# Optimization experiments

Measured on AMD Instinct MI355X. Metric: run time of the kernel, lower is better.

The kernel has to match this reference:

```python
import jax, jax.numpy as jnp
import numpy as np

HIDDEN = 1024
N_HEAD = 16
HEAD_DIM = HIDDEN // N_HEAD  # 64
BATCH = 1
SEQ = 4096
THETA = 10000.0


def _rope_cos_sin(seq_len, head_dim, dtype=jnp.float32):
    # freqs[t, j] = t / theta^(2j/dim), j in [0, dim/2)
    inv_freq = 1.0 / (THETA ** (jnp.arange(0, head_dim, 2, dtype=dtype) / head_dim))
    t = jnp.arange(seq_len, dtype=dtype)
    freqs = jnp.outer(t, inv_freq)           # [S, D/2]
    return jnp.cos(freqs), jnp.sin(freqs)


def _apply_rope(x, cos, sin):
    # x: [B, S, H, D]; pairs (x[...,2j], x[...,2j+1]) rotated by angle freqs[t, j]
    x2 = x.reshape(*x.shape[:-1], -1, 2)       # [B, S, H, D/2, 2]
    x_re, x_im = x2[..., 0], x2[..., 1]
    c = cos[None, :, None, :]                   # [1, S, 1, D/2]
    s = sin[None, :, None, :]
    out_re = x_re * c - x_im * s
    out_im = x_re * s + x_im * c
    out = jnp.stack([out_re, out_im], axis=-1)  # [B, S, H, D/2, 2]
    return out.reshape(x.shape)


def setup_inputs() -> dict:
    key = jax.random.key(0)
    kx, kq, kk, kv = jax.random.split(key, 4)
    scale = 1.0 / np.sqrt(HIDDEN)
    return {
        "x": jax.random.normal(kx, (BATCH, SEQ, HIDDEN), dtype=jnp.float32),
        "wq": jax.random.normal(kq, (HIDDEN, HIDDEN), dtype=jnp.float32) * scale,
        "wk": jax.random.normal(kk, (HIDDEN, HIDDEN), dtype=jnp.float32) * scale,
        "wv": jax.random.normal(kv, (HIDDEN, HIDDEN), dtype=jnp.float32) * scale,
    }


def reference(x, wq, wk, wv):
    B, S, _ = x.shape
    # torch nn.Linear(no bias): y = x @ W.T
    xq = (x @ wq.T).reshape(B, S, N_HEAD, HEAD_DIM).astype(jnp.float32)
    xk = (x @ wk.T).reshape(B, S, N_HEAD, HEAD_DIM).astype(jnp.float32)
    xv = (x @ wv.T).reshape(B, S, N_HEAD, HEAD_DIM).astype(jnp.float32)

    cos, sin = _rope_cos_sin(S, HEAD_DIM)
    q = _apply_rope(xq, cos, sin)
    k = _apply_rope(xk, cos, sin)

    # [B, H, S, S] scores, no causal mask (matches source)
    scores = jnp.einsum("bqhd,bkhd->bhqk", q, k) / jnp.sqrt(
        jnp.asarray(HEAD_DIM, dtype=q.dtype))
    attn = jax.nn.softmax(scores, axis=-1)
    out = jnp.einsum("bhqk,bkhd->bqhd", attn, xv)  # [B, S, H, D]
    return out.reshape(B, S, N_HEAD * HEAD_DIM)
```

## Files before the change

kernel.cpp:

```cpp
#include <hip/hip_runtime.h>
#include <stdint.h>


#define SEQLEN 4096
#define NHEAD 16
#define HDIM 64

typedef __bf16 bf16x8 __attribute__((ext_vector_type(8)));
typedef float f32x4 __attribute__((ext_vector_type(4)));
typedef float f32x16 __attribute__((ext_vector_type(16)));

__device__ __forceinline__ unsigned short f2bf(float f) {
  union { float f; unsigned int u; } v; v.f = f;
  unsigned int r = v.u + 0x7FFFu + ((v.u >> 16) & 1u);
  return (unsigned short)(r >> 16);
}
__device__ __forceinline__ unsigned int pkc(float lo, float hi) {
  union { __bf16 b[2]; unsigned int u; } z;
  z.b[0] = (__bf16)lo; z.b[1] = (__bf16)hi;
  return z.u;
}
__device__ __forceinline__ bf16x8 as_bf(uint4 v) { return __builtin_bit_cast(bf16x8, v); }
__device__ __forceinline__ f32x4 mfma16(bf16x8 a, bf16x8 b, f32x4 c) {
  return __builtin_amdgcn_mfma_f32_16x16x32_bf16(a, b, c, 0, 0, 0);
}
__device__ __forceinline__ f32x16 mfma32(bf16x8 a, bf16x8 b, f32x16 c) {
  return __builtin_amdgcn_mfma_f32_32x32x16_bf16(a, b, c, 0, 0, 0);
}

__global__ __launch_bounds__(256) void k_convert(
    const float* __restrict__ x, const float* __restrict__ wq,
    const float* __restrict__ wk, const float* __restrict__ wv,
    unsigned short* __restrict__ xbf, unsigned short* __restrict__ wbf) {
  int i = blockIdx.x * 256 + threadIdx.x;
  const int NX = SEQLEN * 1024 / 4;
  const int NW = 1024 * 1024 / 4;
  float4 v;
  unsigned short* dst;
  int di;
  if (i < NX) {
    v = ((const float4*)x)[i]; dst = xbf; di = i;
  } else {
    int j = i - NX;
    const float4* src = (const float4*)((j < NW) ? wq : (j < 2 * NW) ? wk : wv);
    v = src[j & (NW - 1)];
    dst = wbf; di = j;
  }
  ushort4 o; o.x = f2bf(v.x); o.y = f2bf(v.y); o.z = f2bf(v.z); o.w = f2bf(v.w);
  ((ushort4*)dst)[di] = o;
}

__global__ __launch_bounds__(256) void k_table(float* __restrict__ ct, float* __restrict__ st) {
  int i = blockIdx.x * 256 + threadIdx.x;
  int s = i >> 5, j = i & 31;
  double inv = exp(-(double)j * 0.28782313662425572);
  double a = (double)s * inv;
  ct[i] = (float)cos(a);
  st[i] = (float)sin(a);
}

__global__ __launch_bounds__(256) void k_gemm(
    const unsigned short* __restrict__ xbf, const unsigned short* __restrict__ wbf,
    const float* __restrict__ ct, const float* __restrict__ st,
    unsigned short* __restrict__ qbf, unsigned short* __restrict__ kbf,
    unsigned short* __restrict__ vT) {
  __shared__ __align__(16) unsigned short As[2][128 * 40];
  __shared__ __align__(16) unsigned short Bs[2][128 * 40];
  const int t = threadIdx.x;
  const int bn = blockIdx.x, bm = blockIdx.y;
  const int lane = t & 63, wave = t >> 6;
  const int r = lane & 15, g = lane >> 4;
  const int wm = wave >> 1, wn = wave & 1;

  const int c0 = t, c1 = t + 256;
  const int ar0 = c0 >> 2, ao0 = (c0 & 3) * 16;
  const int ar1 = c1 >> 2, ao1 = (c1 & 3) * 16;
  const char* Ab = (const char*)xbf;
  const char* Bb = (const char*)wbf;

  uint4 ra0, ra1, rb0, rb1;
#define LD_TILE(kk)                                                             \
  ra0 = *(const uint4*)(Ab + (size_t)(bm * 128 + ar0) * 2048 + (kk) * 64 + ao0); \
  ra1 = *(const uint4*)(Ab + (size_t)(bm * 128 + ar1) * 2048 + (kk) * 64 + ao1); \
  rb0 = *(const uint4*)(Bb + (size_t)(bn * 128 + ar0) * 2048 + (kk) * 64 + ao0); \
  rb1 = *(const uint4*)(Bb + (size_t)(bn * 128 + ar1) * 2048 + (kk) * 64 + ao1);

  LD_TILE(0)
  f32x4 zero4 = {0.f, 0.f, 0.f, 0.f};
  f32x4 acc[4][4];
#pragma unroll
  for (int m = 0; m < 4; ++m)
#pragma unroll
    for (int n = 0; n < 4; ++n) acc[m][n] = zero4;

  for (int kk = 0; kk < 32; ++kk) {
    unsigned short* Ac = As[kk & 1];
    unsigned short* Bc = Bs[kk & 1];
    *(uint4*)((char*)Ac + ar0 * 80 + ao0) = ra0;
    *(uint4*)((char*)Ac + ar1 * 80 + ao1) = ra1;
    *(uint4*)((char*)Bc + ar0 * 80 + ao0) = rb0;
    *(uint4*)((char*)Bc + ar1 * 80 + ao1) = rb1;
    __syncthreads();
    if (kk < 31) { LD_TILE(kk + 1) }
    bf16x8 af[4], bfr[4];
#pragma unroll
    for (int m = 0; m < 4; ++m)
      af[m] = as_bf(*(const uint4*)((const char*)Ac + (wm * 64 + m * 16 + r) * 80 + g * 16));
#pragma unroll
    for (int n = 0; n < 4; ++n)
      bfr[n] = as_bf(*(const uint4*)((const char*)Bc + (wn * 64 + n * 16 + r) * 80 + g * 16));
#pragma unroll
    for (int m = 0; m < 4; ++m)
#pragma unroll
      for (int n = 0; n < 4; ++n)
        acc[m][n] = mfma16(af[m], bfr[n], acc[m][n]);
  }

  const int matid = bn >> 3;
#pragma unroll
  for (int m = 0; m < 4; ++m) {
    const int row0 = bm * 128 + wm * 64 + m * 16 + 4 * g;
#pragma unroll
    for (int n = 0; n < 4; ++n) {
      const int col = bn * 128 + wn * 64 + n * 16 + r;
      const int d = col & 63;
      const int hh = (col >> 6) & 15;
      if (matid < 2) {
        const int jdx = (col >> 1) & 31;
        const float sgn = (col & 1) ? 1.0f : -1.0f;
        unsigned short* dst = (matid == 0) ? qbf : kbf;
        const float qs = (matid == 0) ? 0.18033688011112042f : 1.0f;
#pragma unroll
        for (int j = 0; j < 4; ++j) {
          float v = acc[m][n][j];
          float p = __shfl_xor(v, 1);
          int srow = row0 + j;
          float cv = ct[srow * 32 + jdx];
          float sv = st[srow * 32 + jdx];
          float o = (v * cv + p * sv * sgn) * qs;
          dst[(size_t)srow * 1024 + (hh * 64 + d)] = f2bf(o);
        }
      } else {
        ushort4 o;
        o.x = f2bf(acc[m][n][0]); o.y = f2bf(acc[m][n][1]);
        o.z = f2bf(acc[m][n][2]); o.w = f2bf(acc[m][n][3]);
        *(ushort4*)&vT[((size_t)(hh * 64 + d)) * SEQLEN + row0] = o;
      }
    }
  }
}

__global__ __launch_bounds__(256) void k_attn(
    const unsigned short* __restrict__ qbf, const unsigned short* __restrict__ kbf,
    const unsigned short* __restrict__ vT, float* __restrict__ out) {
  __shared__ __align__(16) char smem[32768];
  const int t = threadIdx.x;
  const int b = blockIdx.x;
  const int work = (b & 7) * 64 + (b >> 3);
  const int h = work >> 5;
  const int qb = work & 31;
  const int lane = t & 63, qw = t >> 6;
  const int li = lane & 31, hi = lane >> 5;
  const int q0 = qb * 128 + qw * 32;

  bf16x8 qf[4];
#pragma unroll
  for (int c = 0; c < 4; ++c)
    qf[c] = as_bf(*(const uint4*)((const char*)qbf +
              (size_t)(q0 + li) * 2048 + h * 128 + c * 32 + hi * 16));

  f32x16 z16 = {0.f};
  f32x16 acc[2];
  acc[0] = z16; acc[1] = z16;
  f32x16 accL = z16;

  uint4 onesu; onesu.x = 0x3F803F80u; onesu.y = 0x3F803F80u;
  onesu.z = 0x3F803F80u; onesu.w = 0x3F803F80u;
  const bf16x8 ones8 = as_bf(onesu);

  const int srow = t >> 2, sbyte = (t & 3) * 16;
  const int swz = (srow & 7) << 4;
  const int wa0 = srow * 128 + (sbyte ^ swz);
  const int wa1 = srow * 128 + ((sbyte + 64) ^ swz);
  const char* kg = (const char*)kbf + h * 128;
  const char* vg = (const char*)vT + (size_t)h * HDIM * SEQLEN * 2;

  uint4 rk0, rk1, rv0, rv1;
#define LD_KV64(kt)                                                            \
  rk0 = *(const uint4*)(kg + (size_t)((kt) * 64 + srow) * 2048 + sbyte);       \
  rk1 = *(const uint4*)(kg + (size_t)((kt) * 64 + srow) * 2048 + sbyte + 64);  \
  rv0 = *(const uint4*)(vg + (size_t)srow * 8192 + (kt) * 128 + sbyte);        \
  rv1 = *(const uint4*)(vg + (size_t)srow * 8192 + (kt) * 128 + sbyte + 64);

  LD_KV64(0)

  const int frsw = (lane & 7) << 4;

  for (int j = 0; j < 64; ++j) {
    char* Kb = smem + (j & 1) * 8192;
    char* Vb = smem + 16384 + (j & 1) * 8192;
    *(uint4*)(Kb + wa0) = rk0;
    *(uint4*)(Kb + wa1) = rk1;
    *(uint4*)(Vb + wa0) = rv0;
    *(uint4*)(Vb + wa1) = rv1;
    __syncthreads();
    if (j < 63) { LD_KV64(j + 1) }

    f32x16 sT[2];
    sT[0] = z16; sT[1] = z16;
    __builtin_amdgcn_s_setprio(1);
#pragma unroll
    for (int c = 0; c < 4; ++c) {
      const int co = (((2 * c + hi) * 16) ^ frsw);
      bf16x8 k0 = as_bf(*(const uint4*)(Kb + li * 128 + co));
      bf16x8 k1 = as_bf(*(const uint4*)(Kb + (32 + li) * 128 + co));
      sT[0] = mfma32(k0, qf[c], sT[0]);
      sT[1] = mfma32(k1, qf[c], sT[1]);
    }
    __builtin_amdgcn_s_setprio(0);

    bf16x8 vf[2][4];
#pragma unroll
    for (int dt = 0; dt < 2; ++dt) {
      const int vrow = (dt * 32 + li) * 128;
#pragma unroll
      for (int kc = 0; kc < 4; ++kc) {
        uint2 vlo = *(const uint2*)(Vb + vrow + (((kc * 32) ^ frsw) + hi * 8));
        uint2 vhi = *(const uint2*)(Vb + vrow + (((kc * 32 + 16) ^ frsw) + hi * 8));
        uint4 vv; vv.x = vlo.x; vv.y = vlo.y; vv.z = vhi.x; vv.w = vhi.y;
        vf[dt][kc] = as_bf(vv);
      }
    }

#pragma unroll
    for (int s = 0; s < 2; ++s)
#pragma unroll
      for (int i = 0; i < 16; ++i) sT[s][i] = __builtin_amdgcn_exp2f(sT[s][i]);

    bf16x8 pfr[4];
#pragma unroll
    for (int kc = 0; kc < 4; ++kc) {
      const int sub = kc >> 1, bix = (kc & 1) * 8;
      uint4 bw;
      bw.x = pkc(sT[sub][bix + 0], sT[sub][bix + 1]);
      bw.y = pkc(sT[sub][bix + 2], sT[sub][bix + 3]);
      bw.z = pkc(sT[sub][bix + 4], sT[sub][bix + 5]);
      bw.w = pkc(sT[sub][bix + 6], sT[sub][bix + 7]);
      pfr[kc] = as_bf(bw);
    }
    __builtin_amdgcn_s_setprio(1);
#pragma unroll
    for (int kc = 0; kc < 4; ++kc) {
      acc[0] = mfma32(vf[0][kc], pfr[kc], acc[0]);
      acc[1] = mfma32(vf[1][kc], pfr[kc], acc[1]);
      accL = mfma32(ones8, pfr[kc], accL);
    }
    __builtin_amdgcn_s_setprio(0);
  }

  float linv = 1.0f / accL[0];

  __syncthreads();
  float* eb = (float*)smem + qw * 1056;
#pragma unroll
  for (int dt = 0; dt < 2; ++dt) {
#pragma unroll
    for (int i = 0; i < 16; ++i)
      eb[li * 33 + ((i & 3) + 8 * (i >> 2) + 4 * hi)] = acc[dt][i] * linv;
    __asm__ volatile("" ::: "memory");
#pragma unroll
    for (int it = 0; it < 16; ++it) {
      int q = it * 2 + hi;
      float v = eb[q * 33 + li];
      out[(size_t)(q0 + q) * 1024 + h * 64 + dt * 32 + li] = v;
    }
    __asm__ volatile("" ::: "memory");
  }
}

extern "C" void kernel_launch(void* const* d_in, const int* in_sizes, int n_in,
                              void* d_out, int out_size, void* d_ws, size_t ws_size,
                              hipStream_t stream) {
  const float* x  = (const float*)d_in[0];
  const float* wq = (const float*)d_in[1];
  const float* wk = (const float*)d_in[2];
  const float* wv = (const float*)d_in[3];
  float* out = (float*)d_out;
  char* ws = (char*)d_ws;

  unsigned short* qbf = (unsigned short*)(ws);
  unsigned short* kbf = (unsigned short*)(ws + ((size_t)8 << 20));
  unsigned short* vT  = (unsigned short*)(ws + ((size_t)16 << 20));
  unsigned short* xbf = (unsigned short*)(ws + ((size_t)24 << 20));
  unsigned short* wbf = (unsigned short*)(ws + ((size_t)32 << 20));
  float* ct = (float*)(ws + ((size_t)38 << 20));
  float* st = (float*)(ws + ((size_t)38 << 20) + ((size_t)512 << 10));

  k_convert<<<dim3(7168), dim3(256), 0, stream>>>(x, wq, wk, wv, xbf, wbf);
  k_table<<<dim3(512), dim3(256), 0, stream>>>(ct, st);
  k_gemm<<<dim3(24, 32), dim3(256), 0, stream>>>(xbf, wbf, ct, st, qbf, kbf, vT);
  k_attn<<<dim3(512), dim3(256), 0, stream>>>(qbf, kbf, vT, out);
}
```

Measured before the change: 170.3 us.

## Split attention KV range in two halves and combine partials in a new kernel

Each attention block now handles only half of the key/value sequence, which doubles the grid from 512 to 1024 blocks. Each half writes an unnormalized output tile and its row sums to workspace. A new elementwise kernel adds the two partials and divides by the summed denominators. The aim is more blocks per CU and better latency hiding, at the cost of an extra launch and extra global traffic to write and re-read the partial outputs.

```diff
diff --git a/kernel.cpp b/kernel.cpp
--- a/kernel.cpp
+++ b/kernel.cpp
@@ -152,13 +152,15 @@
 
 __global__ __launch_bounds__(256) void k_attn(
     const unsigned short* __restrict__ qbf, const unsigned short* __restrict__ kbf,
-    const unsigned short* __restrict__ vT, float* __restrict__ out) {
+    const unsigned short* __restrict__ vT, float* __restrict__ po0,
+    float* __restrict__ out, float* __restrict__ pl) {
   __shared__ __align__(16) char smem[32768];
   const int t = threadIdx.x;
   const int b = blockIdx.x;
-  const int work = (b & 7) * 64 + (b >> 3);
-  const int h = work >> 5;
-  const int qb = work & 31;
+  const int work = (b & 7) * 128 + (b >> 3);
+  const int h = work >> 6;
+  const int qb = (work >> 1) & 31;
+  const int hf = work & 1;
   const int lane = t & 63, qw = t >> 6;
   const int li = lane & 31, hi = lane >> 5;
   const int q0 = qb * 128 + qw * 32;
@@ -192,11 +194,11 @@
   rv0 = *(const uint4*)(vg + (size_t)srow * 8192 + (kt) * 128 + sbyte);        \
   rv1 = *(const uint4*)(vg + (size_t)srow * 8192 + (kt) * 128 + sbyte + 64);
 
-  LD_KV64(0)
+  LD_KV64(hf * 32)
 
   const int frsw = (lane & 7) << 4;
 
-  for (int j = 0; j < 64; ++j) {
+  for (int j = 0; j < 32; ++j) {
     char* Kb = smem + (j & 1) * 8192;
     char* Vb = smem + 16384 + (j & 1) * 8192;
     *(uint4*)(Kb + wa0) = rk0;
@@ -204,7 +206,7 @@
     *(uint4*)(Vb + wa0) = rv0;
     *(uint4*)(Vb + wa1) = rv1;
     __syncthreads();
-    if (j < 63) { LD_KV64(j + 1) }
+    if (j < 31) { LD_KV64(hf * 32 + j + 1) }
 
     f32x16 sT[2];
     sT[0] = z16; sT[1] = z16;
@@ -258,7 +260,8 @@
     __builtin_amdgcn_s_setprio(0);
   }
 
-  float linv = 1.0f / accL[0];
+  float* pout = hf ? out : po0;
+  if (hi == 0) pl[hf * 65536 + h * 4096 + q0 + li] = accL[0];
 
   __syncthreads();
   float* eb = (float*)smem + qw * 1056;
@@ -266,16 +269,33 @@
   for (int dt = 0; dt < 2; ++dt) {
 #pragma unroll
     for (int i = 0; i < 16; ++i)
-      eb[li * 33 + ((i & 3) + 8 * (i >> 2) + 4 * hi)] = acc[dt][i] * linv;
+      eb[li * 33 + ((i & 3) + 8 * (i >> 2) + 4 * hi)] = acc[dt][i];
     __asm__ volatile("" ::: "memory");
 #pragma unroll
     for (int it = 0; it < 16; ++it) {
       int q = it * 2 + hi;
       float v = eb[q * 33 + li];
-      out[(size_t)(q0 + q) * 1024 + h * 64 + dt * 32 + li] = v;
+      pout[(size_t)(q0 + q) * 1024 + h * 64 + dt * 32 + li] = v;
     }
     __asm__ volatile("" ::: "memory");
   }
+}
+
+__global__ __launch_bounds__(256) void k_combine(
+    const float* __restrict__ po, const float* __restrict__ pl,
+    float* __restrict__ out) {
+  int i = blockIdx.x * 256 + threadIdx.x;
+  int flat = i << 2;
+  int q = flat >> 10;
+  int h = (flat >> 6) & 15;
+  float l = pl[h * 4096 + q] + pl[65536 + h * 4096 + q];
+  float linv = 1.0f / l;
+  float4 o = ((const float4*)out)[i];
+  float4 p = ((const float4*)po)[i];
+  float4 r;
+  r.x = (o.x + p.x) * linv; r.y = (o.y + p.y) * linv;
+  r.z = (o.z + p.z) * linv; r.w = (o.w + p.w) * linv;
+  ((float4*)out)[i] = r;
 }
 
 extern "C" void kernel_launch(void* const* d_in, const int* in_sizes, int n_in,
@@ -295,9 +315,12 @@
   unsigned short* wbf = (unsigned short*)(ws + ((size_t)32 << 20));
   float* ct = (float*)(ws + ((size_t)38 << 20));
   float* st = (float*)(ws + ((size_t)38 << 20) + ((size_t)512 << 10));
+  float* po0 = (float*)(ws + ((size_t)24 << 20));
+  float* pl  = (float*)(ws + ((size_t)40 << 20));
 
   k_convert<<<dim3(7168), dim3(256), 0, stream>>>(x, wq, wk, wv, xbf, wbf);
   k_table<<<dim3(512), dim3(256), 0, stream>>>(ct, st);
   k_gemm<<<dim3(24, 32), dim3(256), 0, stream>>>(xbf, wbf, ct, st, qbf, kbf, vT);
-  k_attn<<<dim3(512), dim3(256), 0, stream>>>(qbf, kbf, vT, out);
-}
+  k_attn<<<dim3(1024), dim3(256), 0, stream>>>(qbf, kbf, vT, po0, out, pl);
+  k_combine<<<dim3(4096), dim3(256), 0, stream>>>(po0, pl, out);
+}
```

Result: slower. 182.3 us (+7.0%).
